# Kernel tuning notes

Measured on AMD Instinct MI355X. Metric: run time of the kernel, lower is better.

Reference implementation:

```python
import jax, jax.numpy as jnp
import numpy as np

TOP_K = 2

def setup_inputs() -> dict:
    key = jax.random.key(0)
    k1, k2, k3, k4 = jax.random.split(key, 4)
    T, H, I, E = 8192, 2048, 4096, 8
    s = 0.02
    return {
        "hidden_states": jax.random.normal(k1, (T, H), dtype=jnp.float32),
        "router_w": jax.random.normal(k2, (E, H), dtype=jnp.float32) * s,
        "ws": jax.random.normal(k3, (E, 2 * I, H), dtype=jnp.float32) * s,  # [gate; up]
        "w2s": jax.random.normal(k4, (E, H, I), dtype=jnp.float32) * s,
    }

def reference(hidden_states, router_w, ws, w2s):
    # Router gating: softmax over experts, top-k, NO renormalization
    logits = hidden_states @ router_w.T              # [T, E]
    probs = jax.nn.softmax(logits, axis=-1)
    topv, topi = jax.lax.top_k(probs, TOP_K)         # [T, K]
    T, E = probs.shape
    I = w2s.shape[2]
    # Dense routing-weight matrix [T, E]; top_k indices are unique per token
    w = jnp.zeros_like(probs).at[jnp.arange(T)[:, None], topi].set(topv)
    out = jnp.zeros_like(hidden_states)
    for e in range(E):  # fixed small expert loop; avoids [T,E,2I] blowup
        gate = hidden_states @ ws[e, :I].T           # [T, I]
        up = hidden_states @ ws[e, I:].T             # [T, I]
        h = jax.nn.silu(gate) * up                   # SwiGLU
        out = out + w[:, e:e + 1] * (h @ w2s[e].T)   # combine
    return out
```

## Files before the change

kernel.cpp:

```cpp
#include <hip/hip_runtime.h>
#include <cstdint>
#include <cstddef>

#define T_TOK 8192
#define HDIM  2048
#define IDIM  4096
#define NEXP  8
#define MAXT  72

typedef __bf16 bf16x8 __attribute__((ext_vector_type(8)));
typedef float  f32x4  __attribute__((ext_vector_type(4)));

#define BARRIER() __builtin_amdgcn_s_barrier()
#define LGKM0()   do { asm volatile("s_waitcnt lgkmcnt(0)" ::: "memory"); __builtin_amdgcn_sched_barrier(0); } while (0)
#define VMW(n)    do { asm volatile("s_waitcnt vmcnt(" #n ")" ::: "memory"); } while (0)
#define PRIO1()   __builtin_amdgcn_s_setprio(1)
#define PRIO0()   __builtin_amdgcn_s_setprio(0)

__device__ __forceinline__ unsigned short f2bf(float f) {
    union { float f; unsigned u; } v; v.f = f;
    unsigned r = v.u + 0x7FFFu + ((v.u >> 16) & 1u);
    return (unsigned short)(r >> 16);
}

__device__ __forceinline__ void gload16(const void* g, void* l) {
    __builtin_amdgcn_global_load_lds((__attribute__((address_space(1))) void*)g,
                                     (__attribute__((address_space(3))) void*)l,
                                     16, 0, 0);
}

__global__ __launch_bounds__(256) void router_k(const float* __restrict__ hs,
                                                const float* __restrict__ rw,
                                                float* __restrict__ wgt,
                                                int* __restrict__ counts,
                                                int* __restrict__ lists) {
    int gid  = blockIdx.x * 256 + threadIdx.x;
    int tok  = gid >> 6;
    int lane = threadIdx.x & 63;
    const float* x = hs + (size_t)tok * HDIM;

    float acc[NEXP];
#pragma unroll
    for (int e = 0; e < NEXP; ++e) acc[e] = 0.f;
    for (int h = lane; h < HDIM; h += 64) {
        float xv = x[h];
#pragma unroll
        for (int e = 0; e < NEXP; ++e) acc[e] = fmaf(xv, rw[e * HDIM + h], acc[e]);
    }
#pragma unroll
    for (int off = 32; off > 0; off >>= 1) {
#pragma unroll
        for (int e = 0; e < NEXP; ++e) acc[e] += __shfl_xor(acc[e], off, 64);
    }
    if (lane == 0) {
        float m = acc[0];
#pragma unroll
        for (int e = 1; e < NEXP; ++e) m = fmaxf(m, acc[e]);
        float p[NEXP]; float s = 0.f;
#pragma unroll
        for (int e = 0; e < NEXP; ++e) { p[e] = expf(acc[e] - m); s += p[e]; }
        float inv = 1.f / s;
        int i1 = 0;
#pragma unroll
        for (int e = 1; e < NEXP; ++e) if (acc[e] > acc[i1]) i1 = e;
        int i2 = -1;
#pragma unroll
        for (int e = 0; e < NEXP; ++e) if (e != i1 && (i2 < 0 || acc[e] > acc[i2])) i2 = e;
#pragma unroll
        for (int e = 0; e < NEXP; ++e)
            wgt[(size_t)tok * NEXP + e] = (e == i1 || e == i2) ? p[e] * inv : 0.f;
        int p1 = atomicAdd(&counts[i1], 1);
        lists[i1 * T_TOK + p1] = tok;
        int p2 = atomicAdd(&counts[i2], 1);
        lists[i2 * T_TOK + p2] = (1 << 16) | tok;
    }
}

__global__ void plan_k(const int* __restrict__ counts, int* __restrict__ offs,
                       int* __restrict__ desc, int* __restrict__ ntiles) {
    if (threadIdx.x == 0 && blockIdx.x == 0) {
        int off = 0, n = 0;
        for (int e = 0; e < NEXP; ++e) {
            offs[e] = off;
            int nt = (counts[e] + 255) >> 8;
            for (int t = 0; t < nt; ++t) desc[n++] = (e << 16) | t;
            off += nt * 256;
        }
        *ntiles = n;
    }
}

__global__ __launch_bounds__(256) void cvt_k(const float* __restrict__ in,
                                             unsigned short* __restrict__ out, long n4) {
    long i      = (long)blockIdx.x * 256 + threadIdx.x;
    long stride = (long)gridDim.x * 256;
    const float4* in4 = (const float4*)in;
    ushort4* out4 = (ushort4*)out;
    for (long j = i; j < n4; j += stride) {
        float4 v = in4[j];
        ushort4 o;
        o.x = f2bf(v.x); o.y = f2bf(v.y); o.z = f2bf(v.z); o.w = f2bf(v.w);
        out4[j] = o;
    }
}

__global__ __launch_bounds__(512, 2) void gemm1_k(const unsigned short* __restrict__ A,
                                                  const unsigned short* __restrict__ Wall,
                                                  unsigned short* __restrict__ Hout,
                                                  const int* __restrict__ lists,
                                                  const int* __restrict__ counts,
                                                  const int* __restrict__ offs,
                                                  const int* __restrict__ desc,
                                                  const int* __restrict__ ntiles) {
    const int slot = blockIdx.y;
    if (slot >= *ntiles) return;
    const int dsc = desc[slot];
    const int e = dsc >> 16, tt = dsc & 0xFFFF;
    const int cnt = counts[e];
    const int t0 = tt * 256;
    const int* list = lists + e * T_TOK;
    const unsigned short* W = Wall + (size_t)e * 2 * IDIM * HDIM;
    const int hbase = offs[e];
    const int n0 = blockIdx.x * 128;

    extern __shared__ __align__(16) char lds[];

    const int tid  = threadIdx.x;
    const int lane = tid & 63;
    const int wid  = tid >> 6;
    const int wr   = wid >> 2;
    const int wc   = wid & 3;

    const int prow = tid >> 3;
    const int pcol = (tid & 7) * 16;
    const int lcol = (pcol ^ ((prow & 7) << 4)) >> 1;
    unsigned aoff[4];
#pragma unroll
    for (int i = 0; i < 4; ++i) {
        int g = t0 + i * 64 + prow;
        int tok = list[(g < cnt) ? g : t0] & 0xFFFF;
        aoff[i] = (unsigned)tok * HDIM + lcol;
    }
    unsigned goff[2], uoff[2];
#pragma unroll
    for (int i = 0; i < 2; ++i) {
        goff[i] = (unsigned)(n0 + i * 64 + prow) * HDIM + lcol;
        uoff[i] = (unsigned)(IDIM + n0 + i * 64 + prow) * HDIM + lcol;
    }
    const int dst = tid * 16;

#define G1_STAGE(buf, kt) do {                                                     \
    unsigned k0_ = (unsigned)(kt) * 64;                                            \
    _Pragma("unroll") for (int i_ = 0; i_ < 4; ++i_)                               \
        gload16(A + aoff[i_] + k0_, lds + (buf) * 32768 + i_ * 8192 + dst);        \
    _Pragma("unroll") for (int i_ = 0; i_ < 2; ++i_)                               \
        gload16(W + goff[i_] + k0_, lds + 65536 + (buf) * 16384 + i_ * 8192 + dst);\
    _Pragma("unroll") for (int i_ = 0; i_ < 2; ++i_)                               \
        gload16(W + uoff[i_] + k0_, lds + 98304 + (buf) * 16384 + i_ * 8192 + dst);\
} while (0)

    const int frd = (lane & 7) << 4;
    const int cb0 = (((lane >> 4) * 16)     ) ^ frd;
    const int cb1 = (((lane >> 4) * 16) | 64) ^ frd;
    const int arow = wr * 16384 + (lane & 15) * 128;
    const int brow = (wc * 32 + (lane & 15)) * 128;

    f32x4 accg[8][2], accu[8][2];
#pragma unroll
    for (int mi = 0; mi < 8; ++mi)
#pragma unroll
        for (int ni = 0; ni < 2; ++ni) {
            accg[mi][ni] = (f32x4){0.f, 0.f, 0.f, 0.f};
            accu[mi][ni] = (f32x4){0.f, 0.f, 0.f, 0.f};
        }

    G1_STAGE(0, 0);
    G1_STAGE(1, 1);
    VMW(8);
    BARRIER();

    const int NT = HDIM / 64;
    int buf = 0;
    for (int kt = 0; kt < NT; ++kt) {
        const char* la = lds + buf * 32768 + arow;
        const char* lg = lds + 65536 + buf * 16384 + brow;
        const char* lu = lds + 98304 + buf * 16384 + brow;
        bf16x8 af[4], bg[2], bu[2];
#pragma unroll
        for (int mi = 0; mi < 4; ++mi) af[mi] = *(const bf16x8*)(la + mi * 2048 + cb0);
#pragma unroll
        for (int ni = 0; ni < 2; ++ni) {
            bg[ni] = *(const bf16x8*)(lg + ni * 2048 + cb0);
            bu[ni] = *(const bf16x8*)(lu + ni * 2048 + cb0);
        }
        LGKM0(); PRIO1();
#pragma unroll
        for (int mi = 0; mi < 4; ++mi)
#pragma unroll
            for (int ni = 0; ni < 2; ++ni) {
                accg[mi][ni] = __builtin_amdgcn_mfma_f32_16x16x32_bf16(af[mi], bg[ni], accg[mi][ni], 0, 0, 0);
                accu[mi][ni] = __builtin_amdgcn_mfma_f32_16x16x32_bf16(af[mi], bu[ni], accu[mi][ni], 0, 0, 0);
            }
        PRIO0();
#pragma unroll
        for (int mi = 0; mi < 4; ++mi) af[mi] = *(const bf16x8*)(la + (mi + 4) * 2048 + cb0);
        LGKM0(); PRIO1();
#pragma unroll
        for (int mi = 0; mi < 4; ++mi)
#pragma unroll
            for (int ni = 0; ni < 2; ++ni) {
                accg[mi + 4][ni] = __builtin_amdgcn_mfma_f32_16x16x32_bf16(af[mi], bg[ni], accg[mi + 4][ni], 0, 0, 0);
                accu[mi + 4][ni] = __builtin_amdgcn_mfma_f32_16x16x32_bf16(af[mi], bu[ni], accu[mi + 4][ni], 0, 0, 0);
            }
        PRIO0();
#pragma unroll
        for (int mi = 0; mi < 4; ++mi) af[mi] = *(const bf16x8*)(la + mi * 2048 + cb1);
#pragma unroll
        for (int ni = 0; ni < 2; ++ni) {
            bg[ni] = *(const bf16x8*)(lg + ni * 2048 + cb1);
            bu[ni] = *(const bf16x8*)(lu + ni * 2048 + cb1);
        }
        LGKM0(); PRIO1();
#pragma unroll
        for (int mi = 0; mi < 4; ++mi)
#pragma unroll
            for (int ni = 0; ni < 2; ++ni) {
                accg[mi][ni] = __builtin_amdgcn_mfma_f32_16x16x32_bf16(af[mi], bg[ni], accg[mi][ni], 0, 0, 0);
                accu[mi][ni] = __builtin_amdgcn_mfma_f32_16x16x32_bf16(af[mi], bu[ni], accu[mi][ni], 0, 0, 0);
            }
        PRIO0();
#pragma unroll
        for (int mi = 0; mi < 4; ++mi) af[mi] = *(const bf16x8*)(la + (mi + 4) * 2048 + cb1);
        LGKM0();
        BARRIER();
        G1_STAGE(buf, (kt + 2) & (NT - 1));
        PRIO1();
#pragma unroll
        for (int mi = 0; mi < 4; ++mi)
#pragma unroll
            for (int ni = 0; ni < 2; ++ni) {
                accg[mi + 4][ni] = __builtin_amdgcn_mfma_f32_16x16x32_bf16(af[mi], bg[ni], accg[mi + 4][ni], 0, 0, 0);
                accu[mi + 4][ni] = __builtin_amdgcn_mfma_f32_16x16x32_bf16(af[mi], bu[ni], accu[mi + 4][ni], 0, 0, 0);
            }
        PRIO0();
        VMW(8);
        BARRIER();
        buf ^= 1;
    }
    VMW(0);
#undef G1_STAGE

#pragma unroll
    for (int mi = 0; mi < 8; ++mi)
#pragma unroll
        for (int ni = 0; ni < 2; ++ni)
#pragma unroll
            for (int j = 0; j < 4; ++j) {
                int row = hbase + t0 + wr * 128 + mi * 16 + ((lane >> 4) << 2) + j;
                int col = n0 + wc * 32 + ni * 16 + (lane & 15);
                float g = accg[mi][ni][j], u = accu[mi][ni][j];
                float hv = (g / (1.f + expf(-g))) * u;
                Hout[(size_t)row * IDIM + col] = f2bf(hv);
            }
}

__global__ __launch_bounds__(512, 4) void gemm2_k(const unsigned short* __restrict__ Ah,
                                                  const unsigned short* __restrict__ Ball,
                                                  const float* __restrict__ wgt,
                                                  float* __restrict__ outP,
                                                  const int* __restrict__ lists,
                                                  const int* __restrict__ counts,
                                                  const int* __restrict__ offs,
                                                  const int* __restrict__ desc,
                                                  const int* __restrict__ ntiles) {
    const int slot = blockIdx.y;
    if (slot >= *ntiles) return;
    const int dsc = desc[slot];
    const int e = dsc >> 16, tt = dsc & 0xFFFF;
    const int cnt = counts[e];
    const int t0 = tt * 256;
    const int* list = lists + e * T_TOK;
    const unsigned short* B = Ball + (size_t)e * HDIM * IDIM;
    const int hbase = offs[e];
    const int n0 = blockIdx.x * 128;

    __shared__ __align__(16) char lds[49152];

    const int tid  = threadIdx.x;
    const int lane = tid & 63;
    const int wid  = tid >> 6;
    const int wr   = wid >> 1;
    const int wc   = wid & 1;

    const int prow = tid >> 2;
    const int pcol = (tid & 3) * 16;
    const int lcol = (pcol ^ (((prow >> 1) & 3) << 4)) >> 1;
    const unsigned aoff0 = (unsigned)(hbase + t0 + prow) * IDIM + lcol;
    const unsigned aoff1 = (unsigned)(hbase + t0 + 128 + prow) * IDIM + lcol;
    const unsigned boff  = (unsigned)(n0 + prow) * IDIM + lcol;
    const int dst = tid * 16;

#define G2_STAGE(buf, kt) do {                                        \
    unsigned k0_ = (unsigned)(kt) * 32;                               \
    gload16(Ah + aoff0 + k0_, lds + (buf) * 16384 + dst);             \
    gload16(Ah + aoff1 + k0_, lds + (buf) * 16384 + 8192 + dst);      \
    gload16(B + boff + k0_, lds + 32768 + (buf) * 8192 + dst);        \
} while (0)

    const int cb = ((lane >> 4) << 4) ^ (((lane >> 1) & 3) << 4);
    const int arow = wr * 4096 + (lane & 15) * 64;
    const int brow = wc * 4096 + (lane & 15) * 64;

    f32x4 acc[4][4];
#pragma unroll
    for (int mi = 0; mi < 4; ++mi)
#pragma unroll
        for (int ni = 0; ni < 4; ++ni) acc[mi][ni] = (f32x4){0.f, 0.f, 0.f, 0.f};

    G2_STAGE(0, 0);
    G2_STAGE(1, 1);
    VMW(3);
    BARRIER();

    const int NT = IDIM / 32;
    int buf = 0;
    for (int kt = 0; kt < NT; ++kt) {
        const char* la = lds + buf * 16384 + arow;
        const char* lb = lds + 32768 + buf * 8192 + brow;
        bf16x8 af[4], bfr[4];
#pragma unroll
        for (int mi = 0; mi < 4; ++mi) af[mi] = *(const bf16x8*)(la + mi * 1024 + cb);
#pragma unroll
        for (int ni = 0; ni < 4; ++ni) bfr[ni] = *(const bf16x8*)(lb + ni * 1024 + cb);
        LGKM0(); PRIO1();
#pragma unroll
        for (int mi = 0; mi < 4; ++mi)
#pragma unroll
            for (int ni = 0; ni < 2; ++ni)
                acc[mi][ni] = __builtin_amdgcn_mfma_f32_16x16x32_bf16(af[mi], bfr[ni], acc[mi][ni], 0, 0, 0);
        PRIO0();
        BARRIER();
        G2_STAGE(buf, (kt + 2) & (NT - 1));
        PRIO1();
#pragma unroll
        for (int mi = 0; mi < 4; ++mi)
#pragma unroll
            for (int ni = 2; ni < 4; ++ni)
                acc[mi][ni] = __builtin_amdgcn_mfma_f32_16x16x32_bf16(af[mi], bfr[ni], acc[mi][ni], 0, 0, 0);
        PRIO0();
        VMW(3);
        BARRIER();
        buf ^= 1;
    }
    VMW(0);
#undef G2_STAGE

#pragma unroll
    for (int mi = 0; mi < 4; ++mi)
#pragma unroll
        for (int j = 0; j < 4; ++j) {
            int g = t0 + wr * 64 + mi * 16 + ((lane >> 4) << 2) + j;
            if (g < cnt) {
                int ent = list[g];
                int tok = ent & 0xFFFF;
                int sl  = ent >> 16;
                float w = wgt[(size_t)tok * NEXP + e];
                float* o = outP + (size_t)sl * T_TOK * HDIM + (size_t)tok * HDIM;
#pragma unroll
                for (int ni = 0; ni < 4; ++ni) {
                    int col = n0 + wc * 64 + ni * 16 + (lane & 15);
                    o[col] = w * acc[mi][ni][j];
                }
            }
        }
}

__global__ __launch_bounds__(256) void combine_k(const float* __restrict__ p0,
                                                 const float* __restrict__ p1,
                                                 float* __restrict__ out, long n4) {
    long i      = (long)blockIdx.x * 256 + threadIdx.x;
    long stride = (long)gridDim.x * 256;
    const float4* a4 = (const float4*)p0;
    const float4* b4 = (const float4*)p1;
    float4* o4 = (float4*)out;
    for (long j = i; j < n4; j += stride) {
        float4 a = a4[j], b = b4[j];
        o4[j] = make_float4(a.x + b.x, a.y + b.y, a.z + b.z, a.w + b.w);
    }
}

extern "C" void kernel_launch(void* const* d_in, const int* in_sizes, int n_in,
                              void* d_out, int out_size, void* d_ws, size_t ws_size,
                              hipStream_t stream) {
    const float* hs  = (const float*)d_in[0];
    const float* rw  = (const float*)d_in[1];
    const float* ws  = (const float*)d_in[2];
    const float* w2s = (const float*)d_in[3];
    float* out = (float*)d_out;

    char* wsp = (char*)d_ws;
    unsigned short* hs_bf = (unsigned short*)(wsp);
    unsigned short* w_bf  = (unsigned short*)(wsp + 33554432ULL);
    unsigned short* w2_bf = (unsigned short*)(wsp + 301989888ULL);
    unsigned short* h_bf  = (unsigned short*)(wsp + 436207616ULL);
    float*          outP  = (float*)(wsp + 587202560ULL);
    float*          wgt   = (float*)(wsp + 721420288ULL);
    int*            counts = (int*)(wsp + 721682432ULL);
    int*            offs   = (int*)(wsp + 721682560ULL);
    int*            lists  = (int*)(wsp + 721682688ULL);
    int*            desc   = (int*)(wsp + 721944832ULL);
    int*            ntiles = (int*)(wsp + 721945344ULL);

    hipMemsetAsync(counts, 0, NEXP * sizeof(int), stream);
    cvt_k<<<2048, 256, 0, stream>>>(hs, hs_bf, (long)T_TOK * HDIM / 4);
    cvt_k<<<4096, 256, 0, stream>>>(ws, w_bf, (long)NEXP * 2 * IDIM * HDIM / 4);
    cvt_k<<<4096, 256, 0, stream>>>(w2s, w2_bf, (long)NEXP * HDIM * IDIM / 4);
    router_k<<<(T_TOK * 64) / 256, 256, 0, stream>>>(hs, rw, wgt, counts, lists);
    plan_k<<<1, 64, 0, stream>>>(counts, offs, desc, ntiles);

    gemm1_k<<<dim3(IDIM / 128, MAXT), 512, 131072, stream>>>(
        hs_bf, w_bf, h_bf, lists, counts, offs, desc, ntiles);
    gemm2_k<<<dim3(HDIM / 128, MAXT), 512, 0, stream>>>(
        h_bf, w2_bf, wgt, outP, lists, counts, offs, desc, ntiles);
    combine_k<<<2048, 256, 0, stream>>>(outP, outP + (size_t)T_TOK * HDIM, out,
                                        (long)T_TOK * HDIM / 4);
}
```

Measured before the change: 1.455 ms.

## Split gemm1 K-loop into four phases with staggered per-operand prefetch

Restructures the gate/up GEMM main loop into four MFMA phases (gate top half, up top half, gate bottom half, up bottom half). Each phase issues the global-to-LDS prefetch for one operand slice, so loads are spread through the iteration instead of arriving in one burst. Wave row ownership changes so each wave covers two 64-row quarters, and the epilogue row mapping is updated to match. The aim is better overlap of memory traffic with MFMA work, at the cost of more barriers per iteration and finer vmcnt accounting.

```diff
diff --git a/kernel.cpp b/kernel.cpp
--- a/kernel.cpp
+++ b/kernel.cpp
@@ -149,20 +149,23 @@
     }
     const int dst = tid * 16;
 
-#define G1_STAGE(buf, kt) do {                                                     \
-    unsigned k0_ = (unsigned)(kt) * 64;                                            \
-    _Pragma("unroll") for (int i_ = 0; i_ < 4; ++i_)                               \
-        gload16(A + aoff[i_] + k0_, lds + (buf) * 32768 + i_ * 8192 + dst);        \
-    _Pragma("unroll") for (int i_ = 0; i_ < 2; ++i_)                               \
-        gload16(W + goff[i_] + k0_, lds + 65536 + (buf) * 16384 + i_ * 8192 + dst);\
-    _Pragma("unroll") for (int i_ = 0; i_ < 2; ++i_)                               \
-        gload16(W + uoff[i_] + k0_, lds + 98304 + (buf) * 16384 + i_ * 8192 + dst);\
-} while (0)
+#define SG_AH0(b, t) do { unsigned k0_ = (unsigned)((t) & 31) * 64;      \
+    gload16(A + aoff[0] + k0_, lds + (b) * 32768 + dst);                 \
+    gload16(A + aoff[1] + k0_, lds + (b) * 32768 + 8192 + dst); } while (0)
+#define SG_AH1(b, t) do { unsigned k0_ = (unsigned)((t) & 31) * 64;      \
+    gload16(A + aoff[2] + k0_, lds + (b) * 32768 + 16384 + dst);         \
+    gload16(A + aoff[3] + k0_, lds + (b) * 32768 + 24576 + dst); } while (0)
+#define SG_G(b, t) do { unsigned k0_ = (unsigned)((t) & 31) * 64;        \
+    gload16(W + goff[0] + k0_, lds + 65536 + (b) * 16384 + dst);         \
+    gload16(W + goff[1] + k0_, lds + 65536 + (b) * 16384 + 8192 + dst); } while (0)
+#define SG_U(b, t) do { unsigned k0_ = (unsigned)((t) & 31) * 64;        \
+    gload16(W + uoff[0] + k0_, lds + 98304 + (b) * 16384 + dst);         \
+    gload16(W + uoff[1] + k0_, lds + 98304 + (b) * 16384 + 8192 + dst); } while (0)
 
     const int frd = (lane & 7) << 4;
     const int cb0 = (((lane >> 4) * 16)     ) ^ frd;
     const int cb1 = (((lane >> 4) * 16) | 64) ^ frd;
-    const int arow = wr * 16384 + (lane & 15) * 128;
+    const int arow = (wr * 64 + (lane & 15)) * 128;
     const int brow = (wc * 32 + (lane & 15)) * 128;
 
     f32x4 accg[8][2], accu[8][2];
@@ -174,81 +177,92 @@
             accu[mi][ni] = (f32x4){0.f, 0.f, 0.f, 0.f};
         }
 
-    G1_STAGE(0, 0);
-    G1_STAGE(1, 1);
-    VMW(8);
+    SG_AH0(0, 0); SG_AH1(0, 0); SG_G(0, 0); SG_U(0, 0);
+    SG_AH0(1, 1); SG_AH1(1, 1); SG_G(1, 1); SG_U(1, 1);
+    VMW(0);
     BARRIER();
 
     const int NT = HDIM / 64;
-    int buf = 0;
     for (int kt = 0; kt < NT; ++kt) {
-        const char* la = lds + buf * 32768 + arow;
-        const char* lg = lds + 65536 + buf * 16384 + brow;
-        const char* lu = lds + 98304 + buf * 16384 + brow;
-        bf16x8 af[4], bg[2], bu[2];
-#pragma unroll
-        for (int mi = 0; mi < 4; ++mi) af[mi] = *(const bf16x8*)(la + mi * 2048 + cb0);
+        const int b  = kt & 1;
+        const int bn = b ^ 1;
+        const char* la = lds + b * 32768 + arow;
+        const char* lg = lds + 65536 + b * 16384 + brow;
+        const char* lu = lds + 98304 + b * 16384 + brow;
+        bf16x8 a0[2][4], bg[2][2], bu[2][2];
+
+        VMW(6);
+#pragma unroll
+        for (int mi = 0; mi < 4; ++mi) {
+            a0[0][mi] = *(const bf16x8*)(la + mi * 2048 + cb0);
+            a0[1][mi] = *(const bf16x8*)(la + mi * 2048 + cb1);
+        }
 #pragma unroll
         for (int ni = 0; ni < 2; ++ni) {
-            bg[ni] = *(const bf16x8*)(lg + ni * 2048 + cb0);
-            bu[ni] = *(const bf16x8*)(lu + ni * 2048 + cb0);
-        }
-        LGKM0(); PRIO1();
-#pragma unroll
-        for (int mi = 0; mi < 4; ++mi)
-#pragma unroll
-            for (int ni = 0; ni < 2; ++ni) {
-                accg[mi][ni] = __builtin_amdgcn_mfma_f32_16x16x32_bf16(af[mi], bg[ni], accg[mi][ni], 0, 0, 0);
-                accu[mi][ni] = __builtin_amdgcn_mfma_f32_16x16x32_bf16(af[mi], bu[ni], accu[mi][ni], 0, 0, 0);
-            }
-        PRIO0();
-#pragma unroll
-        for (int mi = 0; mi < 4; ++mi) af[mi] = *(const bf16x8*)(la + (mi + 4) * 2048 + cb0);
-        LGKM0(); PRIO1();
-#pragma unroll
-        for (int mi = 0; mi < 4; ++mi)
-#pragma unroll
-            for (int ni = 0; ni < 2; ++ni) {
-                accg[mi + 4][ni] = __builtin_amdgcn_mfma_f32_16x16x32_bf16(af[mi], bg[ni], accg[mi + 4][ni], 0, 0, 0);
-                accu[mi + 4][ni] = __builtin_amdgcn_mfma_f32_16x16x32_bf16(af[mi], bu[ni], accu[mi + 4][ni], 0, 0, 0);
-            }
-        PRIO0();
-#pragma unroll
-        for (int mi = 0; mi < 4; ++mi) af[mi] = *(const bf16x8*)(la + mi * 2048 + cb1);
+            bg[0][ni] = *(const bf16x8*)(lg + ni * 2048 + cb0);
+            bg[1][ni] = *(const bf16x8*)(lg + ni * 2048 + cb1);
+        }
+        SG_AH1(bn, kt + 1);
+        BARRIER(); LGKM0(); PRIO1();
+#pragma unroll
+        for (int ks = 0; ks < 2; ++ks)
+#pragma unroll
+            for (int mi = 0; mi < 4; ++mi)
+#pragma unroll
+                for (int ni = 0; ni < 2; ++ni)
+                    accg[mi][ni] = __builtin_amdgcn_mfma_f32_16x16x32_bf16(a0[ks][mi], bg[ks][ni], accg[mi][ni], 0, 0, 0);
+        PRIO0(); BARRIER();
+
+        VMW(6);
 #pragma unroll
         for (int ni = 0; ni < 2; ++ni) {
-            bg[ni] = *(const bf16x8*)(lg + ni * 2048 + cb1);
-            bu[ni] = *(const bf16x8*)(lu + ni * 2048 + cb1);
-        }
-        LGKM0(); PRIO1();
-#pragma unroll
-        for (int mi = 0; mi < 4; ++mi)
-#pragma unroll
-            for (int ni = 0; ni < 2; ++ni) {
-                accg[mi][ni] = __builtin_amdgcn_mfma_f32_16x16x32_bf16(af[mi], bg[ni], accg[mi][ni], 0, 0, 0);
-                accu[mi][ni] = __builtin_amdgcn_mfma_f32_16x16x32_bf16(af[mi], bu[ni], accu[mi][ni], 0, 0, 0);
-            }
-        PRIO0();
-#pragma unroll
-        for (int mi = 0; mi < 4; ++mi) af[mi] = *(const bf16x8*)(la + (mi + 4) * 2048 + cb1);
-        LGKM0();
-        BARRIER();
-        G1_STAGE(buf, (kt + 2) & (NT - 1));
+            bu[0][ni] = *(const bf16x8*)(lu + ni * 2048 + cb0);
+            bu[1][ni] = *(const bf16x8*)(lu + ni * 2048 + cb1);
+        }
+        SG_U(bn, kt + 1);
+        BARRIER(); LGKM0(); PRIO1();
+#pragma unroll
+        for (int ks = 0; ks < 2; ++ks)
+#pragma unroll
+            for (int mi = 0; mi < 4; ++mi)
+#pragma unroll
+                for (int ni = 0; ni < 2; ++ni)
+                    accu[mi][ni] = __builtin_amdgcn_mfma_f32_16x16x32_bf16(a0[ks][mi], bu[ks][ni], accu[mi][ni], 0, 0, 0);
+        PRIO0(); BARRIER();
+
+        VMW(6);
+#pragma unroll
+        for (int mi = 0; mi < 4; ++mi) {
+            a0[0][mi] = *(const bf16x8*)(la + 16384 + mi * 2048 + cb0);
+            a0[1][mi] = *(const bf16x8*)(la + 16384 + mi * 2048 + cb1);
+        }
+        SG_AH0(b, kt + 2);
+        BARRIER(); LGKM0(); PRIO1();
+#pragma unroll
+        for (int ks = 0; ks < 2; ++ks)
+#pragma unroll
+            for (int mi = 0; mi < 4; ++mi)
+#pragma unroll
+                for (int ni = 0; ni < 2; ++ni)
+                    accg[mi + 4][ni] = __builtin_amdgcn_mfma_f32_16x16x32_bf16(a0[ks][mi], bg[ks][ni], accg[mi + 4][ni], 0, 0, 0);
+        PRIO0(); BARRIER();
+
+        SG_G(b, kt + 2);
         PRIO1();
 #pragma unroll
-        for (int mi = 0; mi < 4; ++mi)
-#pragma unroll
-            for (int ni = 0; ni < 2; ++ni) {
-                accg[mi + 4][ni] = __builtin_amdgcn_mfma_f32_16x16x32_bf16(af[mi], bg[ni], accg[mi + 4][ni], 0, 0, 0);
-                accu[mi + 4][ni] = __builtin_amdgcn_mfma_f32_16x16x32_bf16(af[mi], bu[ni], accu[mi + 4][ni], 0, 0, 0);
-            }
-        PRIO0();
-        VMW(8);
-        BARRIER();
-        buf ^= 1;
+        for (int ks = 0; ks < 2; ++ks)
+#pragma unroll
+            for (int mi = 0; mi < 4; ++mi)
+#pragma unroll
+                for (int ni = 0; ni < 2; ++ni)
+                    accu[mi + 4][ni] = __builtin_amdgcn_mfma_f32_16x16x32_bf16(a0[ks][mi], bu[ks][ni], accu[mi + 4][ni], 0, 0, 0);
+        PRIO0(); BARRIER();
     }
     VMW(0);
-#undef G1_STAGE
+#undef SG_AH0
+#undef SG_AH1
+#undef SG_G
+#undef SG_U
 
 #pragma unroll
     for (int mi = 0; mi < 8; ++mi)
@@ -256,7 +270,8 @@
         for (int ni = 0; ni < 2; ++ni)
 #pragma unroll
             for (int j = 0; j < 4; ++j) {
-                int row = hbase + t0 + wr * 128 + mi * 16 + ((lane >> 4) << 2) + j;
+                int qr = mi >> 2, m = mi & 3;
+                int row = hbase + t0 + qr * 128 + wr * 64 + m * 16 + ((lane >> 4) << 2) + j;
                 int col = n0 + wc * 32 + ni * 16 + (lane & 15);
                 float g = accg[mi][ni][j], u = accu[mi][ni][j];
                 float hv = (g / (1.f + expf(-g))) * u;
```

Result: faster. 1.399 ms (-3.8%).
